# Performance work log

Measured on AMD Instinct MI355X. Metric: run time of the kernel, lower is better.

## Reference

```python
import jax, jax.numpy as jnp
import numpy as np

B, T, IMG = 64, 20, 64
IN_DIM = IMG * IMG          # 4096, from x.view(B,-1,64*64)
C_IN = 8                    # input_channels
R_DIM = C_IN * 1024         # 8192, reshape(B,20,-1,32,32) constraint
NF = 64                     # num_filters
Z_DIM = 256
LIN_IN = 2 * NF * 7 * 7     # 6272


def setup_inputs() -> dict:
    key = jax.random.key(0)
    ks = jax.random.split(key, 10)
    x = jax.random.normal(ks[0], (B, T, IMG, IMG), jnp.float32)
    Win = jax.random.normal(ks[1], (IN_DIM, R_DIM), jnp.float32) / np.sqrt(IN_DIM).astype(np.float32)
    U = jax.random.normal(ks[2], (IN_DIM, R_DIM), jnp.float32) / np.sqrt(IN_DIM).astype(np.float32)
    Wr = jax.random.normal(ks[3], (R_DIM, R_DIM), jnp.float32) / np.sqrt(R_DIM).astype(np.float32)
    conv1_w = jax.random.normal(ks[4], (NF, C_IN, 3, 3, 3), jnp.float32) * 0.05
    conv1_b = jax.random.normal(ks[5], (NF,), jnp.float32) * 0.01
    conv2_w = jax.random.normal(ks[6], (2 * NF, NF, 3, 4, 4), jnp.float32) * 0.05
    conv2_b = jax.random.normal(ks[7], (2 * NF,), jnp.float32) * 0.01
    lin_w = jax.random.normal(ks[8], (Z_DIM, LIN_IN), jnp.float32) * 0.02
    lin_b = jax.random.normal(ks[9], (Z_DIM,), jnp.float32) * 0.01
    return {"x": x, "Win": Win, "U": U, "Wr": Wr,
            "conv1_w": conv1_w, "conv1_b": conv1_b,
            "conv2_w": conv2_w, "conv2_b": conv2_b,
            "lin_w": lin_w, "lin_b": lin_b}


def reference(x, Win, U, Wr, conv1_w, conv1_b, conv2_w, conv2_b, lin_w, lin_b):
    Bn = x.shape[0]
    xf = x.reshape(Bn, T, IN_DIM)                      # (B,T,4096)
    h0 = jnp.tanh(xf[:, 0] @ Win)                      # (B,R)
    xU = jnp.einsum('bti,ir->tbr', xf[:, 1:], U)       # precompute input drive (T-1,B,R)

    def step(h, xu):
        h = jnp.tanh(xu + h @ Wr)
        return h, h

    _, hs = jax.lax.scan(step, h0, xU)                 # (T-1,B,R)
    H = jnp.concatenate([h0[None], hs], axis=0)        # (T,B,R)
    H = jnp.swapaxes(H, 0, 1)                          # (B,T,R)

    h = H.reshape(Bn, T, C_IN, 32, 32).transpose(0, 2, 1, 3, 4)  # (B,C,T,32,32)
    dn = ('NCDHW', 'OIDHW', 'NCDHW')
    y = jax.lax.conv_general_dilated(h, conv1_w, (1, 2, 2),
                                     [(1, 1), (1, 1), (1, 1)], dimension_numbers=dn)
    y = y + conv1_b[None, :, None, None, None]
    y = jax.nn.leaky_relu(y, 0.01)                     # (B,NF,20,16,16)
    y = jax.lax.conv_general_dilated(y, conv2_w, (1, 2, 2),
                                     [(1, 1), (0, 0), (0, 0)], dimension_numbers=dn)
    y = y + conv2_b[None, :, None, None, None]
    y = jax.nn.leaky_relu(y, 0.01)                     # (B,2NF,20,7,7)

    y = y.reshape(Bn, -1, T, LIN_IN)                   # (B,1,20,6272), same row-major view as torch
    y = y @ lin_w.T + lin_b                            # (B,1,20,Z_DIM)
    mu, log_var = jnp.split(y, 2, axis=3)
    return mu, log_var
```

## Files before the change

kernel.cpp:

```cpp
#include <hip/hip_runtime.h>

typedef __bf16 v8bf __attribute__((ext_vector_type(8)));
typedef float  v4f  __attribute__((ext_vector_type(4)));
typedef unsigned short us8 __attribute__((ext_vector_type(8)));

__device__ __forceinline__ float bf2f(unsigned short u) {
    union { unsigned int i; float f; } v; v.i = ((unsigned int)u) << 16; return v.f;
}
__device__ __forceinline__ unsigned short f2bf(float f) {
    union { float f; unsigned int i; } v; v.f = f;
    return (unsigned short)((v.i + 0x7fffu + ((v.i >> 16) & 1u)) >> 16);
}
__device__ __forceinline__ int sw(int b) { return b ^ (((b >> 7) & 7) << 4); }

__global__ __launch_bounds__(256)
void transpose_f32_bf16(const float* __restrict__ src,
                        unsigned short* __restrict__ dst, int K, int N)
{
    __shared__ unsigned short tile[64][72];
    const int tid = threadIdx.x;
    const int c0 = blockIdx.x * 64, r0 = blockIdx.y * 64;
    const int tr = tid >> 2, tc4 = tid & 3;
    const float* sp = src + (size_t)(r0 + tr) * N + c0 + tc4 * 16;
#pragma unroll
    for (int j = 0; j < 4; ++j) {
        v4f f = *reinterpret_cast<const v4f*>(sp + j * 4);
#pragma unroll
        for (int e = 0; e < 4; ++e) tile[tr][tc4 * 16 + j * 4 + e] = f2bf(f[e]);
    }
    __syncthreads();
    const int ow = tid >> 3, och = tid & 7;
#pragma unroll
    for (int p = 0; p < 2; ++p) {
        int orow = p * 32 + ow;
        us8 o;
#pragma unroll
        for (int e = 0; e < 8; ++e) o[e] = tile[och * 8 + e][orow];
        *reinterpret_cast<us8*>(dst + (size_t)(c0 + orow) * K + r0 + och * 8) = o;
    }
}

__global__ __launch_bounds__(256)
void transpose_f32_bf16_tiled(const float* __restrict__ src,
                              unsigned short* __restrict__ dst, int N, int ktiles)
{
    __shared__ unsigned short tile[64][72];
    const int tid = threadIdx.x;
    const int c0 = blockIdx.x * 64, r0 = blockIdx.y * 64;
    const int tr = tid >> 2, tc4 = tid & 3;
    const float* sp = src + (size_t)(r0 + tr) * N + c0 + tc4 * 16;
#pragma unroll
    for (int j = 0; j < 4; ++j) {
        v4f f = *reinterpret_cast<const v4f*>(sp + j * 4);
#pragma unroll
        for (int e = 0; e < 4; ++e) tile[tr][tc4 * 16 + j * 4 + e] = f2bf(f[e]);
    }
    __syncthreads();
    const int ow = tid >> 3, och = tid & 7;
    unsigned short* tb = dst + ((size_t)blockIdx.x * ktiles + blockIdx.y) * 4096;
#pragma unroll
    for (int p = 0; p < 2; ++p) {
        int orow = p * 32 + ow;
        us8 o;
#pragma unroll
        for (int e = 0; e < 8; ++e) o[e] = tile[och * 8 + e][orow];
        *reinterpret_cast<us8*>(tb + orow * 64 + (och ^ (orow & 7)) * 8) = o;
    }
}

__global__ __launch_bounds__(256)
void cvt_x(const float* __restrict__ x, unsigned short* __restrict__ xb)
{
    int i = blockIdx.x * 256 + threadIdx.x;
    if (i >= 655360) return;
    v4f f0 = *reinterpret_cast<const v4f*>(x + (size_t)i * 8);
    v4f f1 = *reinterpret_cast<const v4f*>(x + (size_t)i * 8 + 4);
    us8 o;
#pragma unroll
    for (int e = 0; e < 4; ++e) { o[e] = f2bf(f0[e]); o[4 + e] = f2bf(f1[e]); }
    *reinterpret_cast<us8*>(xb + (size_t)i * 8) = o;
}

template<int BN, bool STORE_BF16, bool AF32, bool BF32>
__global__ __launch_bounds__(256, 2)
void gemm_bt(const void* __restrict__ Ap, int lda_lo, int lda_hi,
             const void* __restrict__ BTp, int ldb,
             void* __restrict__ Cout, int ldc,
             int ksub, long long csplit_stride)
{
    constexpr int FN  = BN / 32;
    constexpr int BCH = BN / 32;
    const int tid = threadIdx.x;
    const int lane = tid & 63, wid = tid >> 6;
    const int wr = wid >> 1, wc = wid & 1;
    const int nt = blockIdx.x, mt = blockIdx.y, kz = blockIdx.z;
    const int n0 = nt * BN;
    const int kstart = kz * ksub;

    __shared__ unsigned short smem[(64 + BN) * 64];
    char* As = reinterpret_cast<char*>(smem);
    char* Bs = reinterpret_cast<char*>(smem + 64 * 64);

    const unsigned short* A16 = (const unsigned short*)Ap;
    const float*          A32 = (const float*)Ap;
    const unsigned short* B16 = (const unsigned short*)BTp;
    const float*          B32 = (const float*)BTp;

    const int arow = AF32 ? (tid >> 2) : (tid >> 3);
    const int aq   = AF32 ? (tid & 3) : (tid & 7);
    const float* Ab32 = A32 + (size_t)arow * lda_lo + (size_t)mt * lda_hi + kstart + aq * 16;
    const unsigned short* Ab16 = A16 + (size_t)arow * lda_lo + (size_t)mt * lda_hi + kstart + aq * 8;
    const int brow = tid >> 3, bq = tid & 7;
    const float* Bb32 = B32 + (size_t)(n0 + brow) * ldb + kstart + bq * 8;
    const unsigned short* Bb16 = B16 + (size_t)(n0 + brow) * ldb + kstart + bq * 8;

    v4f fa[4];
    us8 ra[2];
    v4f fb[BCH][2];
    us8 rb[BCH];

    auto load = [&](int kk) {
        if (AF32) {
#pragma unroll
            for (int j = 0; j < 4; ++j)
                fa[j] = *reinterpret_cast<const v4f*>(Ab32 + kk + j * 4);
        } else {
#pragma unroll
            for (int p = 0; p < 2; ++p)
                ra[p] = *reinterpret_cast<const us8*>(Ab16 + (size_t)(p * 32) * lda_lo + kk);
        }
        if (BF32) {
#pragma unroll
            for (int p = 0; p < BCH; ++p) {
                fb[p][0] = *reinterpret_cast<const v4f*>(Bb32 + (size_t)(p * 32) * ldb + kk);
                fb[p][1] = *reinterpret_cast<const v4f*>(Bb32 + (size_t)(p * 32) * ldb + kk + 4);
            }
        } else {
#pragma unroll
            for (int p = 0; p < BCH; ++p)
                rb[p] = *reinterpret_cast<const us8*>(Bb16 + (size_t)(p * 32) * ldb + kk);
        }
    };
    auto stage = [&]() {
        if (AF32) {
#pragma unroll
            for (int h = 0; h < 2; ++h) {
                us8 v;
#pragma unroll
                for (int e = 0; e < 8; ++e) v[e] = f2bf(fa[h * 2 + (e >> 2)][e & 3]);
                *reinterpret_cast<us8*>(As + arow * 128 + (((aq * 2 + h) * 16) ^ ((arow & 7) << 4))) = v;
            }
        } else {
#pragma unroll
            for (int p = 0; p < 2; ++p)
                *reinterpret_cast<us8*>(As + (arow + p * 32) * 128 + ((aq * 16) ^ ((arow & 7) << 4))) = ra[p];
        }
#pragma unroll
        for (int p = 0; p < BCH; ++p) {
            us8 v;
            if (BF32) {
#pragma unroll
                for (int e = 0; e < 8; ++e) v[e] = f2bf(fb[p][e >> 2][e & 3]);
            } else v = rb[p];
            *reinterpret_cast<us8*>(Bs + (brow + p * 32) * 128 + ((bq * 16) ^ ((brow & 7) << 4))) = v;
        }
    };

    v4f z4 = {0.f, 0.f, 0.f, 0.f};
    v4f acc[2][FN];
#pragma unroll
    for (int i = 0; i < 2; ++i)
#pragma unroll
        for (int j = 0; j < FN; ++j) acc[i][j] = z4;

    const int l15 = lane & 15, l4 = lane >> 4;
    const int nk = ksub / 64;
    load(0);
    for (int it = 0; it < nk; ++it) {
        __syncthreads();
        stage();
        __syncthreads();
        if (it + 1 < nk) load((it + 1) * 64);
#pragma unroll
        for (int ks = 0; ks < 2; ++ks) {
            const int kb = (ks * 32 + l4 * 8) * 2;
            v8bf af[2], bfr[FN];
#pragma unroll
            for (int fm = 0; fm < 2; ++fm) {
                int row = wr * 32 + fm * 16 + l15;
                af[fm] = *reinterpret_cast<const v8bf*>(As + row * 128 + (kb ^ ((row & 7) << 4)));
            }
#pragma unroll
            for (int fn = 0; fn < FN; ++fn) {
                int row = wc * (BN / 2) + fn * 16 + l15;
                bfr[fn] = *reinterpret_cast<const v8bf*>(Bs + row * 128 + (kb ^ ((row & 7) << 4)));
            }
#pragma unroll
            for (int fm = 0; fm < 2; ++fm)
#pragma unroll
                for (int fn = 0; fn < FN; ++fn)
                    acc[fm][fn] = __builtin_amdgcn_mfma_f32_16x16x32_bf16(af[fm], bfr[fn], acc[fm][fn], 0, 0, 0);
        }
    }
    const long long m0 = (long long)mt * 64;
#pragma unroll
    for (int fm = 0; fm < 2; ++fm)
#pragma unroll
        for (int fn = 0; fn < FN; ++fn)
#pragma unroll
            for (int r = 0; r < 4; ++r) {
                long long row = m0 + wr * 32 + fm * 16 + l4 * 4 + r;
                long long col = n0 + wc * (BN / 2) + fn * 16 + l15;
                long long idx = (long long)kz * csplit_stride + row * ldc + col;
                if (STORE_BF16) reinterpret_cast<unsigned short*>(Cout)[idx] = f2bf(acc[fm][fn][r]);
                else            reinterpret_cast<float*>(Cout)[idx]          = acc[fm][fn][r];
            }
}

#define KZ 4
__global__ __launch_bounds__(256, 2)
void scan_step(const unsigned short* __restrict__ A, int lda,
               const unsigned short* __restrict__ BTiles, int ktiles,
               int kper,
               const unsigned short* __restrict__ xu,
               unsigned short* __restrict__ hnext,
               unsigned short* __restrict__ Hbf, int t,
               float* __restrict__ part,
               unsigned int* __restrict__ tickets)
{
    const int tid = threadIdx.x, lane = tid & 63, wid = tid >> 6;
    const int wr = wid >> 1, wc = wid & 1;
    const int nt = blockIdx.x & 127, kz = blockIdx.x >> 7;
    const int n0 = nt * 64, kstart = kz * kper;
    const int l15 = lane & 15, l4 = lane >> 4;
    const int nit = kper >> 6;

    __shared__ unsigned short smem[32768];
    char* base = reinterpret_cast<char*>(smem);

    const int srow = tid >> 3, sq = tid & 7;
    const int gslot = sq ^ (srow & 7);
    const unsigned short* Asrc = A + (size_t)srow * lda + kstart + gslot * 8;
    const unsigned short* Bsrc = BTiles
        + ((size_t)(nt * ktiles + kz * (kper >> 6))) * 4096 + tid * 8;

    auto stage = [&](int buf, int it) {
        char* dA = base + buf * 16384 + wid * 1024;
        char* dB = dA + 8192;
        const int kk = it * 64;
#pragma unroll
        for (int p = 0; p < 2; ++p) {
            __builtin_amdgcn_global_load_lds(
                (const __attribute__((address_space(1))) void*)(Asrc + kk + (size_t)p * 32 * lda),
                (__attribute__((address_space(3))) void*)(dA + p * 4096), 16, 0, 0);
            __builtin_amdgcn_global_load_lds(
                (const __attribute__((address_space(1))) void*)(Bsrc + (size_t)it * 4096 + p * 2048),
                (__attribute__((address_space(3))) void*)(dB + p * 4096), 16, 0, 0);
        }
    };

    v4f acc00 = {0.f, 0.f, 0.f, 0.f};
    v4f acc01 = acc00, acc10 = acc00, acc11 = acc00;

    stage(0, 0); stage(1, 1); stage(2, 2);
    for (int it = 0; it < nit; ++it) {
        const int ahead = nit - 1 - it;
        if (ahead >= 2)      asm volatile("s_waitcnt vmcnt(8)" ::: "memory");
        else if (ahead == 1) asm volatile("s_waitcnt vmcnt(4)" ::: "memory");
        else                 asm volatile("s_waitcnt vmcnt(0)" ::: "memory");
        __builtin_amdgcn_s_barrier();
        __builtin_amdgcn_sched_barrier(0);
        if (it + 3 < nit) stage((it + 3) & 3, it + 3);
        const char* As = base + (it & 3) * 16384;
        const char* Bs = As + 8192;
#pragma unroll
        for (int ks = 0; ks < 2; ++ks) {
            const int kb = (ks * 32 + l4 * 8) * 2;
            v8bf a0, a1, b0, b1;
            { int row = wr * 32 + l15;      a0 = *reinterpret_cast<const v8bf*>(As + row * 128 + (kb ^ ((row & 7) << 4))); }
            { int row = wr * 32 + 16 + l15; a1 = *reinterpret_cast<const v8bf*>(As + row * 128 + (kb ^ ((row & 7) << 4))); }
            { int row = wc * 32 + l15;      b0 = *reinterpret_cast<const v8bf*>(Bs + row * 128 + (kb ^ ((row & 7) << 4))); }
            { int row = wc * 32 + 16 + l15; b1 = *reinterpret_cast<const v8bf*>(Bs + row * 128 + (kb ^ ((row & 7) << 4))); }
            acc00 = __builtin_amdgcn_mfma_f32_16x16x32_bf16(a0, b0, acc00, 0, 0, 0);
            acc01 = __builtin_amdgcn_mfma_f32_16x16x32_bf16(a0, b1, acc01, 0, 0, 0);
            acc10 = __builtin_amdgcn_mfma_f32_16x16x32_bf16(a1, b0, acc10, 0, 0, 0);
            acc11 = __builtin_amdgcn_mfma_f32_16x16x32_bf16(a1, b1, acc11, 0, 0, 0);
        }
    }

    float* mypart = part + (size_t)kz * 524288;
#pragma unroll
    for (int r = 0; r < 4; ++r) {
        int row0 = wr * 32 + l4 * 4 + r;
        int col0 = n0 + wc * 32 + l15;
        mypart[(size_t)row0 * 8192 + col0]             = acc00[r];
        mypart[(size_t)row0 * 8192 + col0 + 16]        = acc01[r];
        mypart[(size_t)(row0 + 16) * 8192 + col0]      = acc10[r];
        mypart[(size_t)(row0 + 16) * 8192 + col0 + 16] = acc11[r];
    }

    __shared__ int lastflag;
    __syncthreads();
    if (tid == 0) {
        unsigned int old = __hip_atomic_fetch_add(&tickets[nt], 1u,
                              __ATOMIC_ACQ_REL, __HIP_MEMORY_SCOPE_AGENT);
        lastflag = (old == KZ - 1);
    }
    __syncthreads();
    if (!lastflag) return;

    const int row = tid >> 2;
    const int c0 = n0 + (tid & 3) * 16;
    float pre[16];
    if (xu) {
        const us8* xp = reinterpret_cast<const us8*>(xu + (size_t)row * 8192 + c0);
        us8 x0 = xp[0], x1 = xp[1];
#pragma unroll
        for (int j = 0; j < 8; ++j) { pre[j] = bf2f(x0[j]); pre[8 + j] = bf2f(x1[j]); }
    } else {
#pragma unroll
        for (int j = 0; j < 16; ++j) pre[j] = 0.f;
    }
#pragma unroll
    for (int z = 0; z < KZ; ++z) {
        const float* pp = part + (size_t)z * 524288 + (size_t)row * 8192 + c0;
#pragma unroll
        for (int q = 0; q < 4; ++q) {
            v4f v = *reinterpret_cast<const v4f*>(pp + q * 4);
#pragma unroll
            for (int e = 0; e < 4; ++e) pre[q * 4 + e] += v[e];
        }
    }
    us8 o0, o1;
#pragma unroll
    for (int j = 0; j < 16; ++j) {
        unsigned short hb = f2bf(tanhf(pre[j]));
        if (j < 8) o0[j] = hb; else o1[j - 8] = hb;
        int col = c0 + j;
        Hbf[(((size_t)row * 20 + t) * 1024 + (col & 1023)) * 8 + (col >> 10)] = hb;
    }
    *reinterpret_cast<us8*>(hnext + (size_t)row * 8192 + c0)     = o0;
    *reinterpret_cast<us8*>(hnext + (size_t)row * 8192 + c0 + 8) = o1;
    if (tid == 0)
        __hip_atomic_store(&tickets[nt], 0u, __ATOMIC_RELAXED, __HIP_MEMORY_SCOPE_AGENT);
}

#define KZ2 8
__global__ __launch_bounds__(256, 4)
void scan_step2(const unsigned short* __restrict__ A, int lda,
                const unsigned short* __restrict__ BTiles, int ktiles,
                int kper,
                const unsigned short* __restrict__ xu,
                unsigned short* __restrict__ hnext,
                unsigned short* __restrict__ Hbf, int t,
                float* __restrict__ part,
                unsigned int* __restrict__ tickets)
{
    const int tid = threadIdx.x, lane = tid & 63, wid = tid >> 6;
    const int wr = wid >> 1, wc = wid & 1;
    const int nt = blockIdx.x & 127, kz = blockIdx.x >> 7;
    const int n0 = nt * 64, kstart = kz * kper;
    const int l15 = lane & 15, l4 = lane >> 4;
    const int nit = kper >> 6;

    __shared__ unsigned short smem[16384];
    char* base = reinterpret_cast<char*>(smem);

    const int srow = tid >> 3, sq = tid & 7;
    const int gslot = sq ^ (srow & 7);
    const unsigned short* Asrc = A + (size_t)srow * lda + kstart + gslot * 8;
    const unsigned short* Bsrc = BTiles
        + ((size_t)(nt * ktiles + kz * (kper >> 6))) * 4096 + tid * 8;

    auto stage = [&](int buf, int it) {
        char* dA = base + buf * 16384 + wid * 1024;
        char* dB = dA + 8192;
        const int kk = it * 64;
#pragma unroll
        for (int p = 0; p < 2; ++p) {
            __builtin_amdgcn_global_load_lds(
                (const __attribute__((address_space(1))) void*)(Asrc + kk + (size_t)p * 32 * lda),
                (__attribute__((address_space(3))) void*)(dA + p * 4096), 16, 0, 0);
            __builtin_amdgcn_global_load_lds(
                (const __attribute__((address_space(1))) void*)(Bsrc + (size_t)it * 4096 + p * 2048),
                (__attribute__((address_space(3))) void*)(dB + p * 4096), 16, 0, 0);
        }
    };

    v4f acc00 = {0.f, 0.f, 0.f, 0.f};
    v4f acc01 = acc00, acc10 = acc00, acc11 = acc00;

    stage(0, 0);
    for (int it = 0; it < nit; ++it) {
        const int cur = it & 1;
        if (it + 1 < nit) {
            stage(cur ^ 1, it + 1);
            asm volatile("s_waitcnt vmcnt(4)" ::: "memory");
        } else {
            asm volatile("s_waitcnt vmcnt(0)" ::: "memory");
        }
        __builtin_amdgcn_s_barrier();
        __builtin_amdgcn_sched_barrier(0);
        const char* As = base + cur * 16384;
        const char* Bs = As + 8192;
#pragma unroll
        for (int ks = 0; ks < 2; ++ks) {
            const int kb = (ks * 32 + l4 * 8) * 2;
            v8bf a0, a1, b0, b1;
            { int row = wr * 32 + l15;      a0 = *reinterpret_cast<const v8bf*>(As + row * 128 + (kb ^ ((row & 7) << 4))); }
            { int row = wr * 32 + 16 + l15; a1 = *reinterpret_cast<const v8bf*>(As + row * 128 + (kb ^ ((row & 7) << 4))); }
            { int row = wc * 32 + l15;      b0 = *reinterpret_cast<const v8bf*>(Bs + row * 128 + (kb ^ ((row & 7) << 4))); }
            { int row = wc * 32 + 16 + l15; b1 = *reinterpret_cast<const v8bf*>(Bs + row * 128 + (kb ^ ((row & 7) << 4))); }
            acc00 = __builtin_amdgcn_mfma_f32_16x16x32_bf16(a0, b0, acc00, 0, 0, 0);
            acc01 = __builtin_amdgcn_mfma_f32_16x16x32_bf16(a0, b1, acc01, 0, 0, 0);
            acc10 = __builtin_amdgcn_mfma_f32_16x16x32_bf16(a1, b0, acc10, 0, 0, 0);
            acc11 = __builtin_amdgcn_mfma_f32_16x16x32_bf16(a1, b1, acc11, 0, 0, 0);
        }
        __builtin_amdgcn_s_barrier();
    }

    float* mypart = part + (size_t)kz * 524288;
#pragma unroll
    for (int r = 0; r < 4; ++r) {
        int row0 = wr * 32 + l4 * 4 + r;
        int col0 = n0 + wc * 32 + l15;
        mypart[(size_t)row0 * 8192 + col0]             = acc00[r];
        mypart[(size_t)row0 * 8192 + col0 + 16]        = acc01[r];
        mypart[(size_t)(row0 + 16) * 8192 + col0]      = acc10[r];
        mypart[(size_t)(row0 + 16) * 8192 + col0 + 16] = acc11[r];
    }

    __shared__ int lastflag;
    __syncthreads();
    if (tid == 0) {
        unsigned int old = __hip_atomic_fetch_add(&tickets[nt], 1u,
                              __ATOMIC_ACQ_REL, __HIP_MEMORY_SCOPE_AGENT);
        lastflag = (old == KZ2 - 1);
    }
    __syncthreads();
    if (!lastflag) return;

    const int row = tid >> 2;
    const int c0 = n0 + (tid & 3) * 16;
    float pre[16];
    {
        const us8* xp = reinterpret_cast<const us8*>(xu + (size_t)row * 8192 + c0);
        us8 x0 = xp[0], x1 = xp[1];
#pragma unroll
        for (int j = 0; j < 8; ++j) { pre[j] = bf2f(x0[j]); pre[8 + j] = bf2f(x1[j]); }
    }
#pragma unroll
    for (int z = 0; z < KZ2; ++z) {
        const float* pp = part + (size_t)z * 524288 + (size_t)row * 8192 + c0;
#pragma unroll
        for (int q = 0; q < 4; ++q) {
            v4f v = *reinterpret_cast<const v4f*>(pp + q * 4);
#pragma unroll
            for (int e = 0; e < 4; ++e) pre[q * 4 + e] += v[e];
        }
    }
    us8 o0, o1;
#pragma unroll
    for (int j = 0; j < 16; ++j) {
        unsigned short hb = f2bf(tanhf(pre[j]));
        if (j < 8) o0[j] = hb; else o1[j - 8] = hb;
        int col = c0 + j;
        Hbf[(((size_t)row * 20 + t) * 1024 + (col & 1023)) * 8 + (col >> 10)] = hb;
    }
    *reinterpret_cast<us8*>(hnext + (size_t)row * 8192 + c0)     = o0;
    *reinterpret_cast<us8*>(hnext + (size_t)row * 8192 + c0 + 8) = o1;
    if (tid == 0)
        __hip_atomic_store(&tickets[nt], 0u, __ATOMIC_RELAXED, __HIP_MEMORY_SCOPE_AGENT);
}

__global__ __launch_bounds__(256)
void cvt_w1(const float* __restrict__ w, unsigned short* __restrict__ o,
            unsigned int* __restrict__ tickets)
{
    if (blockIdx.x == 0 && threadIdx.x < 128) tickets[threadIdx.x] = 0;
    int idx = blockIdx.x * 256 + threadIdx.x;
    if (idx >= 64 * 224) return;
    int co = idx / 224, k = idx % 224;
    int g = k >> 3, ci = k & 7;
    float v = 0.f;
    if (g < 27) {
        int dt = g / 9, rr = g % 9, dy = rr / 3, dx = rr % 3;
        v = w[(((co * 8 + ci) * 3 + dt) * 3 + dy) * 3 + dx];
    }
    o[idx] = f2bf(v);
}
__global__ __launch_bounds__(256)
void cvt_w2(const float* __restrict__ w, unsigned short* __restrict__ o)
{
    int idx = blockIdx.x * 256 + threadIdx.x;
    if (idx >= 128 * 3072) return;
    int co = idx / 3072, k = idx % 3072;
    int g = k >> 6, ci = k & 63;
    int dt = g >> 4, dy = (g >> 2) & 3, dx = g & 3;
    o[idx] = f2bf(w[(((co * 64 + ci) * 3 + dt) * 4 + dy) * 4 + dx]);
}

__global__ __launch_bounds__(256, 2)
void conv1_kernel(const unsigned short* __restrict__ H,
                  const unsigned short* __restrict__ w1,
                  const float* __restrict__ bias,
                  unsigned short* __restrict__ y1)
{
    const int b = blockIdx.x, t = blockIdx.y;
    const int tid = threadIdx.x, lane = tid & 63, wid = tid >> 6;
    __shared__ unsigned short in_s[3 * 33 * 33 * 8];
    __shared__ unsigned short w_s[64 * 224];

    for (int i = tid; i < 13068; i += 256) reinterpret_cast<unsigned int*>(in_s)[i] = 0;
    __syncthreads();
    for (int idx = tid; idx < 3 * 1024; idx += 256) {
        int dt = idx >> 10, rem = idx & 1023;
        int iy = rem >> 5, ix = rem & 31;
        int ts = t + dt - 1;
        if (ts >= 0 && ts < 20) {
            us8 v = *reinterpret_cast<const us8*>(H + (((size_t)b * 20 + ts) * 1024 + rem) * 8);
            int byte = ((dt * 33 + iy + 1) * 33 + (ix + 1)) * 16;
            *reinterpret_cast<us8*>(reinterpret_cast<char*>(in_s) + sw(byte)) = v;
        }
    }
    for (int idx = tid; idx < 64 * 28; idx += 256) {
        int co = idx / 28, j = idx % 28;
        us8 v = *reinterpret_cast<const us8*>(w1 + co * 224 + j * 8);
        *reinterpret_cast<us8*>(reinterpret_cast<char*>(w_s) + sw(co * 448 + j * 16)) = v;
    }
    __syncthreads();

    const int l15 = lane & 15, l4 = lane >> 4;
    const int m_lo = wid * 64 + l15;
    v4f z4 = {0.f, 0.f, 0.f, 0.f};
    v4f acc[4][4];
#pragma unroll
    for (int i = 0; i < 4; ++i)
#pragma unroll
        for (int j = 0; j < 4; ++j) acc[i][j] = z4;

#pragma unroll
    for (int ks = 0; ks < 7; ++ks) {
        int g = ks * 4 + l4;
        int gc = g < 27 ? g : 26;
        int dt = gc / 9, rr = gc % 9, dy = rr / 3, dx = rr % 3;
        v8bf ap[4], aw[4];
#pragma unroll
        for (int fm = 0; fm < 4; ++fm) {
            int m = fm * 16 + m_lo;
            int py = m >> 4, px = m & 15;
            int byte = ((dt * 33 + 2 * py + dy) * 33 + 2 * px + dx) * 16;
            ap[fm] = *reinterpret_cast<const v8bf*>(reinterpret_cast<const char*>(in_s) + sw(byte));
        }
        int kb2 = (ks * 32 + l4 * 8) * 2;
#pragma unroll
        for (int fc = 0; fc < 4; ++fc) {
            int co = fc * 16 + l15;
            aw[fc] = *reinterpret_cast<const v8bf*>(reinterpret_cast<const char*>(w_s) + sw(co * 448 + kb2));
        }
#pragma unroll
        for (int fm = 0; fm < 4; ++fm)
#pragma unroll
            for (int fc = 0; fc < 4; ++fc)
                acc[fm][fc] = __builtin_amdgcn_mfma_f32_16x16x32_bf16(ap[fm], aw[fc], acc[fm][fc], 0, 0, 0);
    }
#pragma unroll
    for (int fm = 0; fm < 4; ++fm)
#pragma unroll
        for (int fc = 0; fc < 4; ++fc)
#pragma unroll
            for (int r = 0; r < 4; ++r) {
                int m  = wid * 64 + fm * 16 + l4 * 4 + r;
                int co = fc * 16 + l15;
                float v = acc[fm][fc][r] + bias[co];
                v = v > 0.f ? v : 0.01f * v;
                y1[(((size_t)b * 20 + t) * 256 + m) * 64 + co] = f2bf(v);
            }
}

__global__ __launch_bounds__(512, 2)
void conv2_kernel(const unsigned short* __restrict__ y1,
                  const unsigned short* __restrict__ w2,
                  const float* __restrict__ bias,
                  unsigned short* __restrict__ y2)
{
    const int b = blockIdx.x, t = blockIdx.y;
    const int tid = threadIdx.x, lane = tid & 63, wid = tid >> 6;
    const int wc = wid >> 1, wr = wid & 1;
    __shared__ unsigned short in_s[256 * 64];
    __shared__ unsigned short w_s[128 * 128];
    const int l15 = lane & 15, l4 = lane >> 4;

    const int m0v = wr * 32 + l15, m1v = m0v + 16;
    const int m0c = m0v < 49 ? m0v : 48, m1c = m1v < 49 ? m1v : 48;
    const int py0 = m0c / 7, px0 = m0c - py0 * 7;
    const int py1 = m1c / 7, px1 = m1c - py1 * 7;

    v4f acc[2][2];
#pragma unroll
    for (int i = 0; i < 2; ++i)
#pragma unroll
        for (int j = 0; j < 2; ++j) acc[i][j] = (v4f){0.f, 0.f, 0.f, 0.f};

    for (int dt = 0; dt < 3; ++dt) {
        int ts = t + dt - 1;
        __syncthreads();
        if (ts < 0 || ts >= 20) continue;
#pragma unroll
        for (int p = 0; p < 4; ++p) {
            int idx = tid + p * 512;
            int slot = idx >> 3, c8 = idx & 7;
            int yy = slot >> 4, xx = slot & 15;
            us8 v = *reinterpret_cast<const us8*>(y1 + (((size_t)b * 20 + ts) * 256 + slot) * 64 + c8 * 8);
            int cell = ((yy & 1) * 2 + (xx & 1)) * 64 + (yy >> 1) * 8 + (xx >> 1);
            int byte = cell * 128 + ((c8 * 16) ^ (((cell ^ (cell >> 3)) & 7) << 4));
            *reinterpret_cast<us8*>(reinterpret_cast<char*>(in_s) + byte) = v;
        }
        for (int kc = 0; kc < 8; ++kc) {
            __syncthreads();
#pragma unroll
            for (int p = 0; p < 4; ++p) {
                int idx = tid + p * 512;
                int co = idx >> 4, j = idx & 15;
                us8 v = *reinterpret_cast<const us8*>(w2 + (size_t)co * 3072 + dt * 1024 + kc * 128 + j * 8);
                *reinterpret_cast<us8*>(reinterpret_cast<char*>(w_s) + co * 256 + ((j * 16) ^ ((co & 7) << 4))) = v;
            }
            __syncthreads();
#pragma unroll
            for (int ks = 0; ks < 4; ++ks) {
                int klocal = ks * 32 + l4 * 8;
                int kk = kc * 128 + klocal;
                int dy = (kk >> 8) & 3, dx = (kk >> 6) & 3, ci0 = kk & 63;
                v8bf aw[2], bp[2];
#pragma unroll
                for (int fc = 0; fc < 2; ++fc) {
                    int co = wc * 32 + fc * 16 + l15;
                    aw[fc] = *reinterpret_cast<const v8bf*>(reinterpret_cast<const char*>(w_s)
                               + co * 256 + ((klocal * 2) ^ ((co & 7) << 4)));
                }
                int plane = ((dy & 1) << 1) | (dx & 1);
                int c0 = plane * 64 + (py0 + (dy >> 1)) * 8 + px0 + (dx >> 1);
                int c1 = plane * 64 + (py1 + (dy >> 1)) * 8 + px1 + (dx >> 1);
                bp[0] = *reinterpret_cast<const v8bf*>(reinterpret_cast<const char*>(in_s)
                          + c0 * 128 + ((ci0 * 2) ^ (((c0 ^ (c0 >> 3)) & 7) << 4)));
                bp[1] = *reinterpret_cast<const v8bf*>(reinterpret_cast<const char*>(in_s)
                          + c1 * 128 + ((ci0 * 2) ^ (((c1 ^ (c1 >> 3)) & 7) << 4)));
#pragma unroll
                for (int fc = 0; fc < 2; ++fc)
#pragma unroll
                    for (int fm = 0; fm < 2; ++fm)
                        acc[fc][fm] = __builtin_amdgcn_mfma_f32_16x16x32_bf16(aw[fc], bp[fm], acc[fc][fm], 0, 0, 0);
            }
        }
    }
#pragma unroll
    for (int fc = 0; fc < 2; ++fc)
#pragma unroll
        for (int fm = 0; fm < 2; ++fm)
#pragma unroll
            for (int r = 0; r < 4; ++r) {
                int co = wc * 32 + fc * 16 + l4 * 4 + r;
                int m  = wr * 32 + fm * 16 + l15;
                if (m < 49) {
                    float v = acc[fc][fm][r] + bias[co];
                    v = v > 0.f ? v : 0.01f * v;
                    y2[(((size_t)b * 128 + co) * 20 + t) * 49 + m] = f2bf(v);
                }
            }
}

__global__ __launch_bounds__(256)
void lin_epi(const float* __restrict__ linC, const float* __restrict__ lb,
             float* __restrict__ out)
{
    int i = blockIdx.x * 256 + threadIdx.x;
    int m = i >> 8, n = i & 255;
    float v = lb[n];
#pragma unroll
    for (int z = 0; z < 7; ++z) v += linC[(size_t)z * 327680 + i];
    size_t o = (n < 128) ? ((size_t)m * 128 + n) : (163840 + (size_t)m * 128 + (n - 128));
    out[o] = v;
}

extern "C" void kernel_launch(void* const* d_in, const int* in_sizes, int n_in,
                              void* d_out, int out_size, void* d_ws, size_t ws_size,
                              hipStream_t stream)
{
    const float* x   = (const float*)d_in[0];
    const float* Win = (const float*)d_in[1];
    const float* U   = (const float*)d_in[2];
    const float* Wr  = (const float*)d_in[3];
    const float* c1w = (const float*)d_in[4];
    const float* c1b = (const float*)d_in[5];
    const float* c2w = (const float*)d_in[6];
    const float* c2b = (const float*)d_in[7];
    const float* lw  = (const float*)d_in[8];
    const float* lb  = (const float*)d_in[9];

    char* ws = (char*)d_ws;
    unsigned short* WrTile = (unsigned short*)(ws);
    unsigned short* xbf  = (unsigned short*)(ws);
    unsigned short* WT   = (unsigned short*)(ws + 134217728ll);
    float*          part16 = (float*)      (ws + 134217728ll);
    unsigned short* y1   = (unsigned short*)(ws + 134217728ll);
    unsigned short* y2   = (unsigned short*)(ws + 176160768ll);
    unsigned short* XALL = (unsigned short*)(ws + 201326592ll);
    unsigned short* Hbf  = (unsigned short*)(ws + 222298112ll);
    unsigned short* hb0  = (unsigned short*)(ws + 243269632ll);
    unsigned short* hb1  = (unsigned short*)(ws + 244318208ll);
    float*          part = (float*)        (ws + 245366784ll);
    float*          linC = (float*)        (ws + 245366784ll);
    unsigned short* w1bf = (unsigned short*)(ws + 254541824ll);
    unsigned short* w2bf = (unsigned short*)(ws + 254570496ll);
    unsigned int*   tick = (unsigned int*) (ws + 255356928ll);
    float*          out  = (float*)d_out;

    cvt_w1<<<56, 256, 0, stream>>>(c1w, w1bf, tick);
    cvt_w2<<<1536, 256, 0, stream>>>(c2w, w2bf);
    cvt_x<<<2560, 256, 0, stream>>>(x, xbf);

    transpose_f32_bf16_tiled<<<dim3(128, 64), 256, 0, stream>>>(Win, WT, 8192, 64);
    scan_step<<<512, 256, 0, stream>>>(xbf, 81920, WT, 64, 1024,
                                       (const unsigned short*)nullptr, hb0, Hbf, 0, part, tick);

    transpose_f32_bf16<<<dim3(128, 64), 256, 0, stream>>>(U, WT, 4096, 8192);
    gemm_bt<128, true, true, false><<<dim3(64, 19, 1), 256, 0, stream>>>(
        x + 4096, 81920, 4096, WT, 4096, XALL + 524288, 8192, 4096, 0ll);

    transpose_f32_bf16_tiled<<<dim3(128, 128), 256, 0, stream>>>(Wr, WrTile, 8192, 128);
    for (int t = 1; t < 20; ++t) {
        const unsigned short* hprev = (t & 1) ? hb0 : hb1;
        unsigned short*       hnext = (t & 1) ? hb1 : hb0;
        scan_step2<<<1024, 256, 0, stream>>>(hprev, 8192, WrTile, 128, 1024,
                                             XALL + (size_t)t * 524288, hnext, Hbf, t, part16, tick);
    }

    conv1_kernel<<<dim3(64, 20), 256, 0, stream>>>(Hbf, w1bf, c1b, y1);
    conv2_kernel<<<dim3(64, 20), 512, 0, stream>>>(y1, w2bf, c2b, y2);

    gemm_bt<128, false, false, true><<<dim3(2, 20, 7), 256, 0, stream>>>(
        y2, 6272, 6272 * 64, lw, 6272, linC, 256, 896, 327680ll);
    lin_epi<<<1280, 256, 0, stream>>>(linC, lb, out);
}
```

Baseline: 1.811 ms.

## Replace per-step scan launches with persistent kernel using fine-grained readiness flags

The 19 separate recurrence-step launches become one persistent kernel of 512 blocks that loops over time. Blocks wait on per-K-slice readiness counters instead of kernel boundaries. The split-K factor drops from 8 to 4 with a 4-stage LDS pipeline, and the partial buffers are double-buffered by time parity. This removes launch and full-grid drain overhead between steps, but it relies on all 512 blocks being co-resident (2 per CU) and risks deadlock if they are not.

```diff
diff --git a/kernel.cpp b/kernel.cpp
--- a/kernel.cpp
+++ b/kernel.cpp
@@ -345,149 +345,166 @@
         __hip_atomic_store(&tickets[nt], 0u, __ATOMIC_RELAXED, __HIP_MEMORY_SCOPE_AGENT);
 }
 
-#define KZ2 8
-__global__ __launch_bounds__(256, 4)
-void scan_step2(const unsigned short* __restrict__ A, int lda,
-                const unsigned short* __restrict__ BTiles, int ktiles,
-                int kper,
-                const unsigned short* __restrict__ xu,
-                unsigned short* __restrict__ hnext,
-                unsigned short* __restrict__ Hbf, int t,
-                float* __restrict__ part,
-                unsigned int* __restrict__ tickets)
+__global__ __launch_bounds__(256, 2)
+void scan_persist2(const unsigned short* __restrict__ WrTiles,
+                   const unsigned short* __restrict__ xall,
+                   unsigned short* __restrict__ hb0,
+                   unsigned short* __restrict__ hb1,
+                   unsigned short* __restrict__ Hbf,
+                   float* __restrict__ part2,
+                   unsigned int* __restrict__ tscan,
+                   unsigned int* __restrict__ ready)
 {
     const int tid = threadIdx.x, lane = tid & 63, wid = tid >> 6;
     const int wr = wid >> 1, wc = wid & 1;
     const int nt = blockIdx.x & 127, kz = blockIdx.x >> 7;
-    const int n0 = nt * 64, kstart = kz * kper;
+    const int n0 = nt * 64, kstart = kz * 2048;
     const int l15 = lane & 15, l4 = lane >> 4;
-    const int nit = kper >> 6;
-
-    __shared__ unsigned short smem[16384];
+
+    __shared__ unsigned short smem[32768];
     char* base = reinterpret_cast<char*>(smem);
 
     const int srow = tid >> 3, sq = tid & 7;
     const int gslot = sq ^ (srow & 7);
-    const unsigned short* Asrc = A + (size_t)srow * lda + kstart + gslot * 8;
-    const unsigned short* Bsrc = BTiles
-        + ((size_t)(nt * ktiles + kz * (kper >> 6))) * 4096 + tid * 8;
-
-    auto stage = [&](int buf, int it) {
-        char* dA = base + buf * 16384 + wid * 1024;
-        char* dB = dA + 8192;
-        const int kk = it * 64;
-#pragma unroll
-        for (int p = 0; p < 2; ++p) {
-            __builtin_amdgcn_global_load_lds(
-                (const __attribute__((address_space(1))) void*)(Asrc + kk + (size_t)p * 32 * lda),
-                (__attribute__((address_space(3))) void*)(dA + p * 4096), 16, 0, 0);
-            __builtin_amdgcn_global_load_lds(
-                (const __attribute__((address_space(1))) void*)(Bsrc + (size_t)it * 4096 + p * 2048),
-                (__attribute__((address_space(3))) void*)(dB + p * 4096), 16, 0, 0);
-        }
-    };
-
-    v4f acc00 = {0.f, 0.f, 0.f, 0.f};
-    v4f acc01 = acc00, acc10 = acc00, acc11 = acc00;
-
-    stage(0, 0);
-    for (int it = 0; it < nit; ++it) {
-        const int cur = it & 1;
-        if (it + 1 < nit) {
-            stage(cur ^ 1, it + 1);
-            asm volatile("s_waitcnt vmcnt(4)" ::: "memory");
-        } else {
-            asm volatile("s_waitcnt vmcnt(0)" ::: "memory");
-        }
-        __builtin_amdgcn_s_barrier();
-        __builtin_amdgcn_sched_barrier(0);
-        const char* As = base + cur * 16384;
-        const char* Bs = As + 8192;
-#pragma unroll
-        for (int ks = 0; ks < 2; ++ks) {
-            const int kb = (ks * 32 + l4 * 8) * 2;
-            v8bf a0, a1, b0, b1;
-            { int row = wr * 32 + l15;      a0 = *reinterpret_cast<const v8bf*>(As + row * 128 + (kb ^ ((row & 7) << 4))); }
-            { int row = wr * 32 + 16 + l15; a1 = *reinterpret_cast<const v8bf*>(As + row * 128 + (kb ^ ((row & 7) << 4))); }
-            { int row = wc * 32 + l15;      b0 = *reinterpret_cast<const v8bf*>(Bs + row * 128 + (kb ^ ((row & 7) << 4))); }
-            { int row = wc * 32 + 16 + l15; b1 = *reinterpret_cast<const v8bf*>(Bs + row * 128 + (kb ^ ((row & 7) << 4))); }
-            acc00 = __builtin_amdgcn_mfma_f32_16x16x32_bf16(a0, b0, acc00, 0, 0, 0);
-            acc01 = __builtin_amdgcn_mfma_f32_16x16x32_bf16(a0, b1, acc01, 0, 0, 0);
-            acc10 = __builtin_amdgcn_mfma_f32_16x16x32_bf16(a1, b0, acc10, 0, 0, 0);
-            acc11 = __builtin_amdgcn_mfma_f32_16x16x32_bf16(a1, b1, acc11, 0, 0, 0);
-        }
-        __builtin_amdgcn_s_barrier();
-    }
-
-    float* mypart = part + (size_t)kz * 524288;
-#pragma unroll
-    for (int r = 0; r < 4; ++r) {
-        int row0 = wr * 32 + l4 * 4 + r;
-        int col0 = n0 + wc * 32 + l15;
-        mypart[(size_t)row0 * 8192 + col0]             = acc00[r];
-        mypart[(size_t)row0 * 8192 + col0 + 16]        = acc01[r];
-        mypart[(size_t)(row0 + 16) * 8192 + col0]      = acc10[r];
-        mypart[(size_t)(row0 + 16) * 8192 + col0 + 16] = acc11[r];
-    }
-
-    __shared__ int lastflag;
-    __syncthreads();
-    if (tid == 0) {
-        unsigned int old = __hip_atomic_fetch_add(&tickets[nt], 1u,
-                              __ATOMIC_ACQ_REL, __HIP_MEMORY_SCOPE_AGENT);
-        lastflag = (old == KZ2 - 1);
-    }
-    __syncthreads();
-    if (!lastflag) return;
-
-    const int row = tid >> 2;
-    const int c0 = n0 + (tid & 3) * 16;
-    float pre[16];
-    {
-        const us8* xp = reinterpret_cast<const us8*>(xu + (size_t)row * 8192 + c0);
-        us8 x0 = xp[0], x1 = xp[1];
-#pragma unroll
-        for (int j = 0; j < 8; ++j) { pre[j] = bf2f(x0[j]); pre[8 + j] = bf2f(x1[j]); }
-    }
-#pragma unroll
-    for (int z = 0; z < KZ2; ++z) {
-        const float* pp = part + (size_t)z * 524288 + (size_t)row * 8192 + c0;
-#pragma unroll
-        for (int q = 0; q < 4; ++q) {
-            v4f v = *reinterpret_cast<const v4f*>(pp + q * 4);
-#pragma unroll
-            for (int e = 0; e < 4; ++e) pre[q * 4 + e] += v[e];
-        }
-    }
-    us8 o0, o1;
-#pragma unroll
-    for (int j = 0; j < 16; ++j) {
-        unsigned short hb = f2bf(tanhf(pre[j]));
-        if (j < 8) o0[j] = hb; else o1[j - 8] = hb;
-        int col = c0 + j;
-        Hbf[(((size_t)row * 20 + t) * 1024 + (col & 1023)) * 8 + (col >> 10)] = hb;
-    }
-    *reinterpret_cast<us8*>(hnext + (size_t)row * 8192 + c0)     = o0;
-    *reinterpret_cast<us8*>(hnext + (size_t)row * 8192 + c0 + 8) = o1;
-    if (tid == 0)
-        __hip_atomic_store(&tickets[nt], 0u, __ATOMIC_RELAXED, __HIP_MEMORY_SCOPE_AGENT);
+    const unsigned short* Bsrc = WrTiles + ((size_t)(nt * 128 + kz * 32)) * 4096 + tid * 8;
+    unsigned int* rdy = ready + kz * 32;
+    unsigned int* rmy = ready + (nt >> 5) * 32;
+
+    for (int t = 1; t < 20; ++t) {
+        const unsigned short* hprev = (t & 1) ? hb0 : hb1;
+        unsigned short*       hnext = (t & 1) ? hb1 : hb0;
+
+        if (t > 1) {
+            if (tid == 0) {
+                const unsigned int tgt = 32u * (unsigned)(t - 1);
+                while (__hip_atomic_load(rdy, __ATOMIC_RELAXED, __HIP_MEMORY_SCOPE_AGENT) < tgt)
+                    __builtin_amdgcn_s_sleep(2);
+                (void)__hip_atomic_load(rdy, __ATOMIC_ACQUIRE, __HIP_MEMORY_SCOPE_AGENT);
+            }
+            __syncthreads();
+        }
+
+        const unsigned short* Asrc = hprev + (size_t)srow * 8192 + kstart + gslot * 8;
+        auto stage = [&](int buf, int it) {
+            char* dA = base + buf * 16384 + wid * 1024;
+            char* dB = dA + 8192;
+            const int kk = it * 64;
+#pragma unroll
+            for (int p = 0; p < 2; ++p) {
+                __builtin_amdgcn_global_load_lds(
+                    (const __attribute__((address_space(1))) void*)(Asrc + kk + (size_t)p * 32 * 8192),
+                    (__attribute__((address_space(3))) void*)(dA + p * 4096), 16, 0, 0);
+                __builtin_amdgcn_global_load_lds(
+                    (const __attribute__((address_space(1))) void*)(Bsrc + (size_t)it * 4096 + p * 2048),
+                    (__attribute__((address_space(3))) void*)(dB + p * 4096), 16, 0, 0);
+            }
+        };
+
+        v4f acc00 = {0.f, 0.f, 0.f, 0.f};
+        v4f acc01 = acc00, acc10 = acc00, acc11 = acc00;
+
+        stage(0, 0); stage(1, 1); stage(2, 2);
+        for (int it = 0; it < 32; ++it) {
+            const int ahead = 31 - it;
+            if (ahead >= 2)      asm volatile("s_waitcnt vmcnt(8)" ::: "memory");
+            else if (ahead == 1) asm volatile("s_waitcnt vmcnt(4)" ::: "memory");
+            else                 asm volatile("s_waitcnt vmcnt(0)" ::: "memory");
+            __builtin_amdgcn_s_barrier();
+            __builtin_amdgcn_sched_barrier(0);
+            if (it + 3 < 32) stage((it + 3) & 3, it + 3);
+            const char* As = base + (it & 3) * 16384;
+            const char* Bs = As + 8192;
+#pragma unroll
+            for (int ks = 0; ks < 2; ++ks) {
+                const int kb = (ks * 32 + l4 * 8) * 2;
+                v8bf a0, a1, b0, b1;
+                { int row = wr * 32 + l15;      a0 = *reinterpret_cast<const v8bf*>(As + row * 128 + (kb ^ ((row & 7) << 4))); }
+                { int row = wr * 32 + 16 + l15; a1 = *reinterpret_cast<const v8bf*>(As + row * 128 + (kb ^ ((row & 7) << 4))); }
+                { int row = wc * 32 + l15;      b0 = *reinterpret_cast<const v8bf*>(Bs + row * 128 + (kb ^ ((row & 7) << 4))); }
+                { int row = wc * 32 + 16 + l15; b1 = *reinterpret_cast<const v8bf*>(Bs + row * 128 + (kb ^ ((row & 7) << 4))); }
+                acc00 = __builtin_amdgcn_mfma_f32_16x16x32_bf16(a0, b0, acc00, 0, 0, 0);
+                acc01 = __builtin_amdgcn_mfma_f32_16x16x32_bf16(a0, b1, acc01, 0, 0, 0);
+                acc10 = __builtin_amdgcn_mfma_f32_16x16x32_bf16(a1, b0, acc10, 0, 0, 0);
+                acc11 = __builtin_amdgcn_mfma_f32_16x16x32_bf16(a1, b1, acc11, 0, 0, 0);
+            }
+        }
+
+        float* mypart = part2 + ((size_t)((t & 1) * 4 + kz)) * 524288;
+#pragma unroll
+        for (int r = 0; r < 4; ++r) {
+            int row0 = wr * 32 + l4 * 4 + r;
+            int col0 = n0 + wc * 32 + l15;
+            mypart[(size_t)row0 * 8192 + col0]             = acc00[r];
+            mypart[(size_t)row0 * 8192 + col0 + 16]        = acc01[r];
+            mypart[(size_t)(row0 + 16) * 8192 + col0]      = acc10[r];
+            mypart[(size_t)(row0 + 16) * 8192 + col0 + 16] = acc11[r];
+        }
+
+        __shared__ int lastflag;
+        __syncthreads();
+        if (tid == 0) {
+            unsigned int old = __hip_atomic_fetch_add(&tscan[(t - 1) * 128 + nt], 1u,
+                                  __ATOMIC_ACQ_REL, __HIP_MEMORY_SCOPE_AGENT);
+            lastflag = (old == 3u);
+        }
+        __syncthreads();
+        if (lastflag) {
+            const int row = tid >> 2;
+            const int c0 = n0 + (tid & 3) * 16;
+            const unsigned short* xu = xall + (size_t)t * 524288;
+            float pre[16];
+            {
+                const us8* xp = reinterpret_cast<const us8*>(xu + (size_t)row * 8192 + c0);
+                us8 x0 = xp[0], x1 = xp[1];
+#pragma unroll
+                for (int j = 0; j < 8; ++j) { pre[j] = bf2f(x0[j]); pre[8 + j] = bf2f(x1[j]); }
+            }
+            const float* pbase = part2 + (size_t)(t & 1) * 4 * 524288;
+#pragma unroll
+            for (int z = 0; z < 4; ++z) {
+                const float* pp = pbase + (size_t)z * 524288 + (size_t)row * 8192 + c0;
+#pragma unroll
+                for (int q = 0; q < 4; ++q) {
+                    v4f v = *reinterpret_cast<const v4f*>(pp + q * 4);
+#pragma unroll
+                    for (int e = 0; e < 4; ++e) pre[q * 4 + e] += v[e];
+                }
+            }
+            us8 o0, o1;
+#pragma unroll
+            for (int j = 0; j < 16; ++j) {
+                unsigned short hb = f2bf(tanhf(pre[j]));
+                if (j < 8) o0[j] = hb; else o1[j - 8] = hb;
+                int col = c0 + j;
+                Hbf[(((size_t)row * 20 + t) * 1024 + (col & 1023)) * 8 + (col >> 10)] = hb;
+            }
+            *reinterpret_cast<us8*>(hnext + (size_t)row * 8192 + c0)     = o0;
+            *reinterpret_cast<us8*>(hnext + (size_t)row * 8192 + c0 + 8) = o1;
+            __syncthreads();
+            if (tid == 0)
+                __hip_atomic_fetch_add(rmy, 1u, __ATOMIC_ACQ_REL, __HIP_MEMORY_SCOPE_AGENT);
+        }
+    }
 }
 
 __global__ __launch_bounds__(256)
 void cvt_w1(const float* __restrict__ w, unsigned short* __restrict__ o,
-            unsigned int* __restrict__ tickets)
-{
-    if (blockIdx.x == 0 && threadIdx.x < 128) tickets[threadIdx.x] = 0;
-    int idx = blockIdx.x * 256 + threadIdx.x;
-    if (idx >= 64 * 224) return;
-    int co = idx / 224, k = idx % 224;
+            unsigned int* __restrict__ tickets,
+            unsigned int* __restrict__ tscan,
+            unsigned int* __restrict__ ready)
+{
+    int gi = blockIdx.x * 256 + threadIdx.x;
+    if (gi < 2432) tscan[gi] = 0;
+    if (gi < 128)  { tickets[gi] = 0; ready[gi] = 0; }
+    if (gi >= 64 * 224) return;
+    int co = gi / 224, k = gi % 224;
     int g = k >> 3, ci = k & 7;
     float v = 0.f;
     if (g < 27) {
         int dt = g / 9, rr = g % 9, dy = rr / 3, dx = rr % 3;
         v = w[(((co * 8 + ci) * 3 + dt) * 3 + dy) * 3 + dx];
     }
-    o[idx] = f2bf(v);
+    o[gi] = f2bf(v);
 }
 __global__ __launch_bounds__(256)
 void cvt_w2(const float* __restrict__ w, unsigned short* __restrict__ o)
@@ -701,7 +718,7 @@
     unsigned short* WrTile = (unsigned short*)(ws);
     unsigned short* xbf  = (unsigned short*)(ws);
     unsigned short* WT   = (unsigned short*)(ws + 134217728ll);
-    float*          part16 = (float*)      (ws + 134217728ll);
+    float*          part2 = (float*)       (ws + 134217728ll);
     unsigned short* y1   = (unsigned short*)(ws + 134217728ll);
     unsigned short* y2   = (unsigned short*)(ws + 176160768ll);
     unsigned short* XALL = (unsigned short*)(ws + 201326592ll);
@@ -713,9 +730,11 @@
     unsigned short* w1bf = (unsigned short*)(ws + 254541824ll);
     unsigned short* w2bf = (unsigned short*)(ws + 254570496ll);
     unsigned int*   tick = (unsigned int*) (ws + 255356928ll);
+    unsigned int*   tscan= (unsigned int*) (ws + 255357440ll);
+    unsigned int*   ready= (unsigned int*) (ws + 255367168ll);
     float*          out  = (float*)d_out;
 
-    cvt_w1<<<56, 256, 0, stream>>>(c1w, w1bf, tick);
+    cvt_w1<<<56, 256, 0, stream>>>(c1w, w1bf, tick, tscan, ready);
     cvt_w2<<<1536, 256, 0, stream>>>(c2w, w2bf);
     cvt_x<<<2560, 256, 0, stream>>>(x, xbf);
 
@@ -728,12 +747,7 @@
         x + 4096, 81920, 4096, WT, 4096, XALL + 524288, 8192, 4096, 0ll);
 
     transpose_f32_bf16_tiled<<<dim3(128, 128), 256, 0, stream>>>(Wr, WrTile, 8192, 128);
-    for (int t = 1; t < 20; ++t) {
-        const unsigned short* hprev = (t & 1) ? hb0 : hb1;
-        unsigned short*       hnext = (t & 1) ? hb1 : hb0;
-        scan_step2<<<1024, 256, 0, stream>>>(hprev, 8192, WrTile, 128, 1024,
-                                             XALL + (size_t)t * 524288, hnext, Hbf, t, part16, tick);
-    }
+    scan_persist2<<<512, 256, 0, stream>>>(WrTile, XALL, hb0, hb1, Hbf, part2, tscan, ready);
 
     conv1_kernel<<<dim3(64, 20), 256, 0, stream>>>(Hbf, w1bf, c1b, y1);
     conv2_kernel<<<dim3(64, 20), 512, 0, stream>>>(y1, w2bf, c2b, y2);
```

Result: faster. 1.637 ms (-9.6%).
